# Kernel tuning notes

Hardware: AMD Instinct MI355X
Metric: run time of the kernel (lower is better)

Reference implementation:

```python
import jax, jax.numpy as jnp
import numpy as np
from jax import lax

V, E, H, B, T = 50000, 512, 512, 128, 256
OUT = 2

def gru(x, Wi, Wh, bi, bh):
    # x: [B,T,D]; PyTorch GRU equations, h0 = 0. Returns all hidden states [B,T,H].
    Bsz = x.shape[0]
    Hd = Wh.shape[1]
    xW = jnp.einsum('btd,gd->btg', x, Wi) + bi  # [B,T,3H], precompute input projections
    def step(h, xw):
        gh = h @ Wh.T + bh
        xr, xz, xn = jnp.split(xw, 3, axis=-1)
        hr, hz, hn = jnp.split(gh, 3, axis=-1)
        r = jax.nn.sigmoid(xr + hr)
        z = jax.nn.sigmoid(xz + hz)
        n = jnp.tanh(xn + r * hn)
        h_new = (1.0 - z) * n + z * h
        return h_new, h_new
    h0 = jnp.zeros((Bsz, Hd), x.dtype)
    _, hs = lax.scan(step, h0, jnp.swapaxes(xW, 0, 1))
    return jnp.swapaxes(hs, 0, 1)

def dual_attention(u, r, u_all_sum, Aw, bw, Ww):
    # u, r: [B,T,D] (query side / response side per timestep, vectorized over T).
    # w_t[b,t] = (u A^T + b) . r  (the original bmm of [B,1,D] x [B,D,1])
    w = jnp.einsum('btd,btd->bt', jnp.einsum('btd,ed->bte', u, Aw) + bw, r)
    # score = softmax over D of tanh(w) * Ww  (Linear(1, D, bias=False))
    sc = jax.nn.softmax(jnp.tanh(w)[..., None] * Ww[None, None, :], axis=-1)  # [B,T,D]
    # sum_s embed[b,s,:] * score[b,t,:] = score * (sum over time) ; then * r_t
    return sc * u_all_sum[:, None, :] * r  # [B,T,D]

def setup_inputs() -> dict:
    key = jax.random.key(0)
    ks = jax.random.split(key, 24)
    d = {}
    d['ask'] = jax.random.randint(ks[0], (B, T), 0, V, dtype=jnp.int32)
    d['answer'] = jax.random.randint(ks[1], (B, T), 0, V, dtype=jnp.int32)
    d['ask_keyword'] = jax.random.randint(ks[2], (B, T), 0, V, dtype=jnp.int32)
    d['answer_keyword'] = jax.random.randint(ks[3], (B, T), 0, V, dtype=jnp.int32)
    d['embed'] = jax.random.normal(ks[4], (V, E), jnp.float32) * 0.02
    # GRU 1: input E -> hidden H
    d['Wi1'] = jax.random.normal(ks[5], (3 * H, E), jnp.float32) * 0.05
    d['Wh1'] = jax.random.normal(ks[6], (3 * H, H), jnp.float32) * 0.05
    d['bi1'] = jnp.zeros((3 * H,), jnp.float32)
    d['bh1'] = jnp.zeros((3 * H,), jnp.float32)
    # word attention: Linear(E,E) + Linear(1,E,bias=False)
    d['Aw'] = jax.random.normal(ks[7], (E, E), jnp.float32) * 0.05
    d['bw'] = jnp.zeros((E,), jnp.float32)
    d['Ww'] = jax.random.normal(ks[8], (E,), jnp.float32) * 0.05
    # seq attention: Linear(H,H) + Linear(1,H,bias=False)
    d['As'] = jax.random.normal(ks[9], (H, H), jnp.float32) * 0.05
    d['bs'] = jnp.zeros((H,), jnp.float32)
    d['Ws'] = jax.random.normal(ks[10], (H,), jnp.float32) * 0.05
    # GRU 2: input E+H -> hidden H
    d['Wi2'] = jax.random.normal(ks[11], (3 * H, E + H), jnp.float32) * 0.05
    d['Wh2'] = jax.random.normal(ks[12], (3 * H, H), jnp.float32) * 0.05
    d['bi2'] = jnp.zeros((3 * H,), jnp.float32)
    d['bh2'] = jnp.zeros((3 * H,), jnp.float32)
    # final classifier
    d['Wf'] = jax.random.normal(ks[13], (OUT, H), jnp.float32) * 0.05
    d['bf'] = jnp.zeros((OUT,), jnp.float32)
    return d

def reference(ask, answer, ask_keyword, answer_keyword, embed, Wi1, Wh1, bi1, bh1,
              Aw, bw, Ww, As, bs, Ws, Wi2, Wh2, bi2, bh2, Wf, bf):
    ask_e = embed[ask]            # [B,T,E]
    ans_e = embed[answer]
    ask_kw = embed[ask_keyword]
    ans_kw = embed[answer_keyword]
    h_ask = gru(ask_e, Wi1, Wh1, bi1, bh1)  # [B,T,H]
    h_ans = gru(ans_e, Wi1, Wh1, bi1, bh1)
    # dual attention, vectorized over the original Python loop over t
    ctx_word = dual_attention(ask_kw, ans_kw, ask_kw.sum(axis=1), Aw, bw, Ww)   # [B,T,E]
    ctx_seq = dual_attention(h_ask, h_ans, h_ask.sum(axis=1), As, bs, Ws)       # [B,T,H]
    v = jnp.concatenate([ctx_word, ctx_seq], axis=-1)  # [B,T,E+H]
    h2 = gru(v, Wi2, Wh2, bi2, bh2)[:, -1, :]  # final hidden state [B,H]
    # dropout is identity in eval mode
    return jax.nn.softmax(h2 @ Wf.T + bf, axis=1)
```

## Files before the change

kernel.cpp:

```cpp
#include <hip/hip_runtime.h>
#include <cstdio>

typedef __bf16 bf16x8 __attribute__((ext_vector_type(8)));
typedef float f32x4 __attribute__((ext_vector_type(4)));

#define DEV __device__ __forceinline__

DEV short f2bf(float f) {
    unsigned u = __builtin_bit_cast(unsigned, f);
    u += 0x7fffu + ((u >> 16) & 1u);
    return (short)(u >> 16);
}
DEV float bf2f(short s) {
    unsigned u = ((unsigned)(unsigned short)s) << 16;
    return __builtin_bit_cast(float, u);
}
DEV float sigmoidf_(float x) { return 1.0f / (1.0f + __expf(-x)); }
DEV float tanhf_(float x) { float e = __expf(2.0f * x); return 1.0f - 2.0f / (e + 1.0f); }

DEV void gload_lds16(const void* g, void* l) {
    __builtin_amdgcn_global_load_lds(
        (__attribute__((address_space(1))) void*)(g),
        (__attribute__((address_space(3))) void*)(l), 16, 0, 0);
}

DEV f32x4 mfma16(bf16x8 a, bf16x8 b, f32x4 c) {
    return __builtin_amdgcn_mfma_f32_16x16x32_bf16(a, b, c, 0, 0, 0);
}

__global__ void f2bf_vec(const float* __restrict__ in, short* __restrict__ out, int n4) {
    int i = blockIdx.x * 256 + threadIdx.x;
    if (i >= n4) return;
    float4 v = reinterpret_cast<const float4*>(in)[i];
    short4 o;
    o.x = f2bf(v.x); o.y = f2bf(v.y); o.z = f2bf(v.z); o.w = f2bf(v.w);
    reinterpret_cast<short4*>(out)[i] = o;
}

__global__ void pack_wh(const float* __restrict__ Wh, short* __restrict__ Wp) {
    int tile = blockIdx.x, kk = blockIdx.y, l = threadIdx.x;
    int n = tile * 16 + (l & 15);
    int k0 = kk * 32 + (l >> 4) * 8;
    const float* src = Wh + (size_t)n * 512 + k0;
    short o[8];
#pragma unroll
    for (int e = 0; e < 8; e++) o[e] = f2bf(src[e]);
    *(int4*)(Wp + ((size_t)(tile * 16 + kk) * 64 + l) * 8) = *(int4*)o;
}

enum { M_XW1 = 0, M_UAW = 1, M_UAS = 2, M_XW2 = 3 };

template<int MODE>
__global__ __launch_bounds__(256) void gemm_bt(
    const short* __restrict__ Abase, const short* __restrict__ A2,
    const int* __restrict__ tok0, const int* __restrict__ tok1,
    const short* __restrict__ W, const float* __restrict__ bias,
    short* __restrict__ C, int M, int N, int K)
{
    __shared__ short Als[128 * 64];
    __shared__ short Bls[128 * 64];
    int tid = threadIdx.x;
    int m0 = blockIdx.y * 128, n0 = blockIdx.x * 128;
    int kc = (tid & 7) * 8;

    const short* arow[4];
#pragma unroll
    for (int i = 0; i < 4; i++) {
        int gm = m0 + i * 32 + (tid >> 3);
        if (MODE == M_XW1) {
            int t = gm >> 8, s = gm & 255;
            int tok = (s < 128) ? tok0[s * 256 + t] : tok1[(s - 128) * 256 + t];
            arow[i] = Abase + (size_t)tok * 512;
        } else if (MODE == M_UAW) {
            int t = gm >> 7, b = gm & 127;
            arow[i] = Abase + (size_t)tok0[b * 256 + t] * 512;
        } else if (MODE == M_UAS) {
            int t = gm >> 7, b = gm & 127;
            arow[i] = Abase + ((size_t)t * 256 + b) * 512;
        } else {
            arow[i] = Abase + (size_t)gm * 512;
        }
    }

    f32x4 acc[4][4] = {};
    int l = tid & 63, w = tid >> 6;
    int wm = (w >> 1) * 64, wn = (w & 1) * 64;

    for (int kt = 0; kt < K; kt += 64) {
#pragma unroll
        for (int i = 0; i < 4; i++) {
            const short* asrc;
            if (MODE == M_XW2) {
                int gm = m0 + i * 32 + (tid >> 3);
                const short* base = (kt < 512) ? Abase : A2;
                asrc = base + (size_t)gm * 512 + (kt & 511) + kc;
            } else {
                asrc = arow[i] + kt + kc;
            }
            gload_lds16(asrc, &Als[i * 2048 + tid * 8]);
        }
#pragma unroll
        for (int i = 0; i < 4; i++) {
            const short* bsrc = W + (size_t)(n0 + i * 32 + (tid >> 3)) * K + kt + kc;
            gload_lds16(bsrc, &Bls[i * 2048 + tid * 8]);
        }
        __syncthreads();
#pragma unroll
        for (int kk = 0; kk < 2; kk++) {
            int ko = kk * 32 + (l >> 4) * 8;
            bf16x8 af[4], bfr[4];
#pragma unroll
            for (int mi = 0; mi < 4; mi++)
                af[mi] = *(const bf16x8*)&Als[(wm + mi * 16 + (l & 15)) * 64 + ko];
#pragma unroll
            for (int ni = 0; ni < 4; ni++)
                bfr[ni] = *(const bf16x8*)&Bls[(wn + ni * 16 + (l & 15)) * 64 + ko];
#pragma unroll
            for (int mi = 0; mi < 4; mi++)
#pragma unroll
                for (int ni = 0; ni < 4; ni++)
                    acc[mi][ni] = mfma16(af[mi], bfr[ni], acc[mi][ni]);
        }
        __syncthreads();
    }
#pragma unroll
    for (int ni = 0; ni < 4; ni++) {
        int col = n0 + wn + ni * 16 + (l & 15);
        float bv = bias[col];
#pragma unroll
        for (int mi = 0; mi < 4; mi++) {
            int row0 = m0 + wm + mi * 16 + (l >> 4) * 4;
#pragma unroll
            for (int j = 0; j < 4; j++)
                C[(size_t)(row0 + j) * N + col] = f2bf(acc[mi][ni][j] + bv);
        }
    }
}

template<int WRITE_ALL>
__global__ __launch_bounds__(256, 1) void gru_scan10(
    const short* __restrict__ xW,
    const short* __restrict__ Wp,
    const float* __restrict__ bh,
    short* __restrict__ hb0, short* __restrict__ hb1,
    short* __restrict__ h_all,
    float* __restrict__ h_final,
    unsigned* __restrict__ done,
    int S, int T)
{
    __shared__ char wl[96 * 1024];
    __shared__ char sl[32 * 1024];
    __shared__ char ho[2048];

    int cb = blockIdx.x;
    int rg = blockIdx.y;
    int r0 = rg * 32;
    int tid = threadIdx.x;
    int w = tid >> 6, l = tid & 63;
    int rt = w >> 1, ct = w & 1;
    int lrow = l & 15, lq = l >> 4;
    int colg = cb * 32 + ct * 16 + lrow;
    unsigned* mydone = done + rg * 32;

    for (int rr = 0; rr < 24; rr++) {
        int flat = rr * 256 + tid;
        int lane = flat & 63, kk = (flat >> 6) & 15, lg = flat >> 10;
        int g = lg >> 1, c2 = lg & 1;
        gload_lds16(Wp + (((size_t)(g * 32 + cb * 2 + c2) * 16 + kk) * 64 + lane) * 8,
                    wl + flat * 16);
    }
    float bhv[3];
#pragma unroll
    for (int g = 0; g < 3; g++) bhv[g] = bh[g * 512 + colg];
    __syncthreads();

    float hp[4] = {};

    for (int t = 0; t < T; t++) {
        short xrv[4], xzv[4], xnv[4];
        const short* xbase = xW + ((size_t)t * S + r0) * 1536 + colg;
#pragma unroll
        for (int j = 0; j < 4; j++) {
            const short* xp = xbase + (size_t)(rt * 16 + lq * 4 + j) * 1536;
            xrv[j] = xp[0]; xzv[j] = xp[512]; xnv[j] = xp[1024];
        }

        f32x4 acc[3] = {};
        if (t > 0) {
            const short* hprev = ((t & 1) ? hb0 : hb1) + (size_t)r0 * 512;
            if (tid < 16) {
                while (__hip_atomic_load(&mydone[tid], __ATOMIC_RELAXED,
                                         __HIP_MEMORY_SCOPE_AGENT) < (unsigned)t)
                    __builtin_amdgcn_s_sleep(1);
            }
            __syncthreads();
            unsigned long long v[16];
            const unsigned long long* sp = (const unsigned long long*)hprev;
#pragma unroll
            for (int k = 0; k < 16; k++)
                v[k] = __hip_atomic_load(sp + k * 256 + tid,
                                         __ATOMIC_RELAXED, __HIP_MEMORY_SCOPE_AGENT);
#pragma unroll
            for (int k = 0; k < 16; k++) {
                int off = (k * 256 + tid) * 8;
                int row = off >> 10, colb = off & 1023;
                *(unsigned long long*)(sl + row * 1024 + (colb ^ ((row & 7) << 4))) = v[k];
            }
            __syncthreads();
            bf16x8 afr[16];
            int ar = rt * 16 + lrow;
#pragma unroll
            for (int kk = 0; kk < 16; kk++) {
                int colb = kk * 64 + lq * 16;
                afr[kk] = *(const bf16x8*)(sl + ar * 1024 + (colb ^ ((ar & 7) << 4)));
            }
#pragma unroll
            for (int g = 0; g < 3; g++) {
                const char* bbase = wl + (size_t)((g * 2 + ct) * 16) * 1024 + l * 16;
#pragma unroll
                for (int kk = 0; kk < 16; kk++) {
                    bf16x8 bfr = *(const bf16x8*)(bbase + kk * 1024);
                    acc[g] = mfma16(afr[kk], bfr, acc[g]);
                }
            }
        }

        float hv[4];
#pragma unroll
        for (int j = 0; j < 4; j++) {
            float r = sigmoidf_(bf2f(xrv[j]) + bhv[0] + acc[0][j]);
            float z = sigmoidf_(bf2f(xzv[j]) + bhv[1] + acc[1][j]);
            float n = tanhf_(bf2f(xnv[j]) + r * (acc[2][j] + bhv[2]));
            hv[j] = (1.f - z) * n + z * hp[j];
            hp[j] = hv[j];
            *(short*)(ho + (rt * 16 + lq * 4 + j) * 64 + (ct * 16 + lrow) * 2) = f2bf(hv[j]);
        }
        __syncthreads();
        {
            int row = tid >> 3, ch = tid & 7;
            unsigned long long val = *(const unsigned long long*)(ho + row * 64 + ch * 8);
            short* hnew = (t & 1) ? hb1 : hb0;
            __hip_atomic_store(
                (unsigned long long*)(hnew + (size_t)(r0 + row) * 512 + cb * 32 + ch * 4),
                val, __ATOMIC_RELAXED, __HIP_MEMORY_SCOPE_AGENT);
            if (WRITE_ALL)
                *(unsigned long long*)(h_all + ((size_t)t * S + r0 + row) * 512 + cb * 32 + ch * 4) = val;
        }
        if (!WRITE_ALL && t == T - 1) {
#pragma unroll
            for (int j = 0; j < 4; j++)
                h_final[(size_t)(r0 + rt * 16 + lq * 4 + j) * 512 + colg] = hv[j];
        }
        __syncthreads();
        if (tid == 0)
            __hip_atomic_store(&mydone[cb], (unsigned)(t + 1),
                               __ATOMIC_RELAXED, __HIP_MEMORY_SCOPE_AGENT);
    }
}

__global__ void embed_sum_k(const short* __restrict__ ebf, const int* __restrict__ tok,
                            float* __restrict__ out) {
    int b = blockIdx.x, d = threadIdx.x;
    float a0 = 0.f, a1 = 0.f;
    for (int t = 0; t < 256; t++) {
        const short* row = ebf + (size_t)tok[b * 256 + t] * 512;
        a0 += bf2f(row[d]); a1 += bf2f(row[d + 256]);
    }
    out[b * 512 + d] = a0; out[b * 512 + d + 256] = a1;
}
__global__ void hall_sum_k(const short* __restrict__ h_all, float* __restrict__ out) {
    int b = blockIdx.x, d = threadIdx.x;
    float a0 = 0.f, a1 = 0.f;
    for (int t = 0; t < 256; t++) {
        const short* row = h_all + ((size_t)t * 256 + b) * 512;
        a0 += bf2f(row[d]); a1 += bf2f(row[d + 256]);
    }
    out[b * 512 + d] = a0; out[b * 512 + d + 256] = a1;
}

template<int WORD>
__global__ __launch_bounds__(256) void attn_combine(
    const short* __restrict__ uA, const short* __restrict__ rsrc,
    const int* __restrict__ rtok, const float* __restrict__ usum,
    const float* __restrict__ Wv, short* __restrict__ ctx)
{
    int l = threadIdx.x & 63, w = threadIdx.x >> 6;
    int m = blockIdx.x * 4 + w;
    int t = m >> 7, b = m & 127;
    const short* rrow;
    if (WORD) rrow = rsrc + (size_t)rtok[b * 256 + t] * 512;
    else      rrow = rsrc + ((size_t)t * 256 + 128 + b) * 512;
    const short* urow = uA + (size_t)m * 512;
    int d0 = l * 8;
    short ru[8], uu[8];
    *(int4*)ru = *(const int4*)(rrow + d0);
    *(int4*)uu = *(const int4*)(urow + d0);
    float rv[8], dot = 0.f;
#pragma unroll
    for (int i = 0; i < 8; i++) { rv[i] = bf2f(ru[i]); dot += rv[i] * bf2f(uu[i]); }
#pragma unroll
    for (int off = 32; off >= 1; off >>= 1) dot += __shfl_xor(dot, off);
    float tw = tanhf_(dot);
    float e[8], se = 0.f;
#pragma unroll
    for (int i = 0; i < 8; i++) { e[i] = __expf(tw * Wv[d0 + i]); se += e[i]; }
#pragma unroll
    for (int off = 32; off >= 1; off >>= 1) se += __shfl_xor(se, off);
    float inv = 1.f / se;
    short ov[8];
#pragma unroll
    for (int i = 0; i < 8; i++) ov[i] = f2bf(e[i] * inv * usum[b * 512 + d0 + i] * rv[i]);
    *(int4*)(ctx + (size_t)m * 512 + d0) = *(int4*)ov;
}

__global__ void final_head_k(const float* __restrict__ h2, const float* __restrict__ Wf,
                             const float* __restrict__ bfv, float* __restrict__ out) {
    int b = blockIdx.x, l = threadIdx.x;
    float d0 = 0.f, d1 = 0.f;
    for (int k = l; k < 512; k += 64) {
        float h = h2[b * 512 + k];
        d0 += h * Wf[k];
        d1 += h * Wf[512 + k];
    }
#pragma unroll
    for (int off = 32; off >= 1; off >>= 1) { d0 += __shfl_xor(d0, off); d1 += __shfl_xor(d1, off); }
    if (l == 0) {
        float l0 = d0 + bfv[0], l1 = d1 + bfv[1];
        float mx = fmaxf(l0, l1);
        float e0 = __expf(l0 - mx), e1 = __expf(l1 - mx);
        float s = e0 + e1;
        out[b * 2] = e0 / s; out[b * 2 + 1] = e1 / s;
    }
}

extern "C" void kernel_launch(void* const* d_in, const int* in_sizes, int n_in,
                              void* d_out, int out_size, void* d_ws, size_t ws_size,
                              hipStream_t stream)
{
    const int* ask    = (const int*)d_in[0];
    const int* answer = (const int*)d_in[1];
    const int* askkw  = (const int*)d_in[2];
    const int* anskw  = (const int*)d_in[3];
    const float* embed = (const float*)d_in[4];
    const float* Wi1 = (const float*)d_in[5];
    const float* Wh1 = (const float*)d_in[6];
    const float* bi1 = (const float*)d_in[7];
    const float* bh1 = (const float*)d_in[8];
    const float* Aw  = (const float*)d_in[9];
    const float* bw  = (const float*)d_in[10];
    const float* Ww  = (const float*)d_in[11];
    const float* As  = (const float*)d_in[12];
    const float* bs  = (const float*)d_in[13];
    const float* Ws  = (const float*)d_in[14];
    const float* Wi2 = (const float*)d_in[15];
    const float* Wh2 = (const float*)d_in[16];
    const float* bi2 = (const float*)d_in[17];
    const float* bh2 = (const float*)d_in[18];
    const float* Wf  = (const float*)d_in[19];
    const float* bfv = (const float*)d_in[20];

    char* ws = (char*)d_ws;
    size_t off = 0;
    auto alloc = [&](size_t bytes) -> void* {
        void* p = (void*)(ws + off);
        off += (bytes + 255) & ~(size_t)255;
        return p;
    };
    short* embed_bf = (short*)alloc(50000ULL * 512 * 2);
    short* Wi1b = (short*)alloc(1536 * 512 * 2);
    short* Wp1  = (short*)alloc(1536 * 512 * 2);
    short* Awb  = (short*)alloc(512 * 512 * 2);
    short* Asb  = (short*)alloc(512 * 512 * 2);
    short* Wi2b = (short*)alloc(1536 * 1024 * 2);
    short* Wp2  = (short*)alloc(1536 * 512 * 2);
    char* X = (char*)alloc(201326592ULL);
    short* xW1  = (short*)X;
    short* uA   = (short*)X;
    short* ctxW = (short*)(X + 33554432);
    short* ctxS = (short*)(X + 67108864);
    short* xW2  = (short*)(X + 100663296);
    short* h_all = (short*)alloc(256ULL * 256 * 512 * 2);
    short* hb0 = (short*)alloc(256 * 512 * 2);
    short* hb1 = (short*)alloc(256 * 512 * 2);
    float* usumW = (float*)alloc(128 * 512 * 4);
    float* usumS = (float*)alloc(128 * 512 * 4);
    float* h2f   = (float*)alloc(128 * 512 * 4);
    unsigned* done1 = (unsigned*)alloc(8 * 32 * 4);
    unsigned* done2 = (unsigned*)alloc(4 * 32 * 4);

    if (off > ws_size) {
        fprintf(stderr, "kernel_launch: workspace too small: need %zu have %zu\n", off, ws_size);
        return;
    }

    hipMemsetAsync(done1, 0, 8 * 32 * 4, stream);
    hipMemsetAsync(done2, 0, 4 * 32 * 4, stream);

    auto cv = [&](const float* src, short* dst, int n) {
        int n4 = n / 4;
        f2bf_vec<<<(n4 + 255) / 256, 256, 0, stream>>>(src, dst, n4);
    };
    cv(embed, embed_bf, 50000 * 512);
    cv(Wi1, Wi1b, 1536 * 512);
    cv(Aw, Awb, 512 * 512);
    cv(As, Asb, 512 * 512);
    cv(Wi2, Wi2b, 1536 * 1024);
    pack_wh<<<dim3(96, 16), 64, 0, stream>>>(Wh1, Wp1);
    pack_wh<<<dim3(96, 16), 64, 0, stream>>>(Wh2, Wp2);

    gemm_bt<M_XW1><<<dim3(12, 512), 256, 0, stream>>>(
        embed_bf, nullptr, ask, answer, Wi1b, bi1, xW1, 65536, 1536, 512);

    {
        const short* xWa = xW1; const short* Wpa = Wp1; const float* bha = bh1;
        short* a0 = hb0; short* a1 = hb1; short* ha = h_all; float* hf = h2f;
        unsigned* dp = done1; int S = 256, T = 256;
        void* args[] = { (void*)&xWa, (void*)&Wpa, (void*)&bha, (void*)&a0, (void*)&a1,
                         (void*)&ha, (void*)&hf, (void*)&dp, (void*)&S, (void*)&T };
        hipError_t e = hipLaunchCooperativeKernel(
            reinterpret_cast<void*>(&gru_scan10<1>), dim3(16, 8), dim3(256), args, 0, stream);
        if (e != hipSuccess)
            gru_scan10<1><<<dim3(16, 8), 256, 0, stream>>>(xWa, Wpa, bha, a0, a1, ha, hf, dp, S, T);
    }

    embed_sum_k<<<128, 256, 0, stream>>>(embed_bf, askkw, usumW);
    gemm_bt<M_UAW><<<dim3(4, 256), 256, 0, stream>>>(
        embed_bf, nullptr, askkw, nullptr, Awb, bw, uA, 32768, 512, 512);
    attn_combine<1><<<8192, 256, 0, stream>>>(uA, embed_bf, anskw, usumW, Ww, ctxW);

    hall_sum_k<<<128, 256, 0, stream>>>(h_all, usumS);
    gemm_bt<M_UAS><<<dim3(4, 256), 256, 0, stream>>>(
        h_all, nullptr, nullptr, nullptr, Asb, bs, uA, 32768, 512, 512);
    attn_combine<0><<<8192, 256, 0, stream>>>(uA, h_all, nullptr, usumS, Ws, ctxS);

    gemm_bt<M_XW2><<<dim3(12, 256), 256, 0, stream>>>(
        ctxW, ctxS, nullptr, nullptr, Wi2b, bi2, xW2, 32768, 1536, 1024);

    {
        const short* xWa = xW2; const short* Wpa = Wp2; const float* bha = bh2;
        short* a0 = hb0; short* a1 = hb1; short* ha = nullptr; float* hf = h2f;
        unsigned* dp = done2; int S = 128, T = 256;
        void* args[] = { (void*)&xWa, (void*)&Wpa, (void*)&bha, (void*)&a0, (void*)&a1,
                         (void*)&ha, (void*)&hf, (void*)&dp, (void*)&S, (void*)&T };
        hipError_t e = hipLaunchCooperativeKernel(
            reinterpret_cast<void*>(&gru_scan10<0>), dim3(16, 4), dim3(256), args, 0, stream);
        if (e != hipSuccess)
            gru_scan10<0><<<dim3(16, 4), 256, 0, stream>>>(xWa, Wpa, bha, a0, a1, ha, hf, dp, S, T);
    }

    final_head_k<<<128, 64, 0, stream>>>(h2f, Wf, bfv, (float*)d_out);
}
```

Baseline: 2.227 ms.

## Fuse input-projection GEMMs and attention into persistent GRU scan kernels

Result: faster. 1.930 ms, median of 2 (-13.3%).

```diff
diff --git a/kernel.cpp b/kernel.cpp
--- a/kernel.cpp
+++ b/kernel.cpp
@@ -23,9 +23,23 @@
         (__attribute__((address_space(1))) void*)(g),
         (__attribute__((address_space(3))) void*)(l), 16, 0, 0);
 }
-
 DEV f32x4 mfma16(bf16x8 a, bf16x8 b, f32x4 c) {
     return __builtin_amdgcn_mfma_f32_16x16x32_bf16(a, b, c, 0, 0, 0);
+}
+DEV unsigned ald(const unsigned* p) {
+    return __hip_atomic_load(p, __ATOMIC_RELAXED, __HIP_MEMORY_SCOPE_AGENT);
+}
+DEV unsigned long long ald64(const void* p) {
+    return __hip_atomic_load((const unsigned long long*)p, __ATOMIC_RELAXED, __HIP_MEMORY_SCOPE_AGENT);
+}
+DEV void ast64(void* p, unsigned long long v) {
+    __hip_atomic_store((unsigned long long*)p, v, __ATOMIC_RELAXED, __HIP_MEMORY_SCOPE_AGENT);
+}
+DEV void ast32(void* p, unsigned v) {
+    __hip_atomic_store((unsigned*)p, v, __ATOMIC_RELAXED, __HIP_MEMORY_SCOPE_AGENT);
+}
+DEV void aadd(unsigned* p, unsigned v) {
+    __hip_atomic_fetch_add(p, v, __ATOMIC_RELAXED, __HIP_MEMORY_SCOPE_AGENT);
 }
 
 __global__ void f2bf_vec(const float* __restrict__ in, short* __restrict__ out, int n4) {
@@ -48,33 +62,31 @@
     *(int4*)(Wp + ((size_t)(tile * 16 + kk) * 64 + l) * 8) = *(int4*)o;
 }
 
-enum { M_XW1 = 0, M_UAW = 1, M_UAS = 2, M_XW2 = 3 };
+enum { A_XW1 = 0, A_UAW = 1, A_UAS = 2, A_XW2 = 3 };
 
 template<int MODE>
-__global__ __launch_bounds__(256) void gemm_bt(
-    const short* __restrict__ Abase, const short* __restrict__ A2,
-    const int* __restrict__ tok0, const int* __restrict__ tok1,
-    const short* __restrict__ W, const float* __restrict__ bias,
-    short* __restrict__ C, int M, int N, int K)
+DEV void gemm_tile(short* Als, short* Bls, short* Ct, int m0, int n0,
+                   const short* Abase, const short* A2,
+                   const int* tok0, const int* tok1,
+                   const short* W, const float* bias, short* C, int N, int K)
 {
-    __shared__ short Als[128 * 64];
-    __shared__ short Bls[128 * 64];
     int tid = threadIdx.x;
-    int m0 = blockIdx.y * 128, n0 = blockIdx.x * 128;
+    int l = tid & 63, w = tid >> 6;
+    int wm = (w >> 1) * 64, wn = (w & 1) * 64;
     int kc = (tid & 7) * 8;
 
     const short* arow[4];
 #pragma unroll
     for (int i = 0; i < 4; i++) {
         int gm = m0 + i * 32 + (tid >> 3);
-        if (MODE == M_XW1) {
+        if (MODE == A_XW1) {
             int t = gm >> 8, s = gm & 255;
             int tok = (s < 128) ? tok0[s * 256 + t] : tok1[(s - 128) * 256 + t];
             arow[i] = Abase + (size_t)tok * 512;
-        } else if (MODE == M_UAW) {
+        } else if (MODE == A_UAW) {
             int t = gm >> 7, b = gm & 127;
             arow[i] = Abase + (size_t)tok0[b * 256 + t] * 512;
-        } else if (MODE == M_UAS) {
+        } else if (MODE == A_UAS) {
             int t = gm >> 7, b = gm & 127;
             arow[i] = Abase + ((size_t)t * 256 + b) * 512;
         } else {
@@ -83,27 +95,23 @@
     }
 
     f32x4 acc[4][4] = {};
-    int l = tid & 63, w = tid >> 6;
-    int wm = (w >> 1) * 64, wn = (w & 1) * 64;
-
     for (int kt = 0; kt < K; kt += 64) {
 #pragma unroll
         for (int i = 0; i < 4; i++) {
             const short* asrc;
-            if (MODE == M_XW2) {
+            if (MODE == A_XW2) {
                 int gm = m0 + i * 32 + (tid >> 3);
                 const short* base = (kt < 512) ? Abase : A2;
                 asrc = base + (size_t)gm * 512 + (kt & 511) + kc;
             } else {
                 asrc = arow[i] + kt + kc;
             }
-            gload_lds16(asrc, &Als[i * 2048 + tid * 8]);
-        }
-#pragma unroll
-        for (int i = 0; i < 4; i++) {
-            const short* bsrc = W + (size_t)(n0 + i * 32 + (tid >> 3)) * K + kt + kc;
-            gload_lds16(bsrc, &Bls[i * 2048 + tid * 8]);
-        }
+            gload_lds16(asrc, Als + i * 2048 + tid * 8);
+        }
+#pragma unroll
+        for (int i = 0; i < 4; i++)
+            gload_lds16(W + (size_t)(n0 + i * 32 + (tid >> 3)) * K + kt + kc,
+                        Bls + i * 2048 + tid * 8);
         __syncthreads();
 #pragma unroll
         for (int kk = 0; kk < 2; kk++) {
@@ -125,37 +133,101 @@
     }
 #pragma unroll
     for (int ni = 0; ni < 4; ni++) {
-        int col = n0 + wn + ni * 16 + (l & 15);
-        float bv = bias[col];
-#pragma unroll
-        for (int mi = 0; mi < 4; mi++) {
-            int row0 = m0 + wm + mi * 16 + (l >> 4) * 4;
-#pragma unroll
-            for (int j = 0; j < 4; j++)
-                C[(size_t)(row0 + j) * N + col] = f2bf(acc[mi][ni][j] + bv);
-        }
+        float bv = bias[n0 + wn + ni * 16 + (l & 15)];
+#pragma unroll
+        for (int mi = 0; mi < 4; mi++)
+#pragma unroll
+            for (int jj = 0; jj < 4; jj++)
+                Ct[(wm + mi * 16 + (l >> 4) * 4 + jj) * 132 + wn + ni * 16 + (l & 15)] =
+                    f2bf(acc[mi][ni][jj] + bv);
+    }
+    __syncthreads();
+    for (int r = 0; r < 16; r++) {
+        int idx = r * 256 + tid;
+        int row = idx >> 5, cc = idx & 31;
+        unsigned long long val = *(const unsigned long long*)(Ct + row * 132 + cc * 4);
+        ast64(C + (size_t)(m0 + row) * N + n0 + cc * 4, val);
+    }
+    __syncthreads();
+}
+
+DEV void embed_sum_dev(const short* ebf, const int* tok, float* out, int b) {
+    int d = threadIdx.x;
+    float a0 = 0.f, a1 = 0.f;
+    for (int t = 0; t < 256; t++) {
+        const short* row = ebf + (size_t)tok[b * 256 + t] * 512;
+        a0 += bf2f(row[d]); a1 += bf2f(row[d + 256]);
+    }
+    ast32(&out[b * 512 + d], __builtin_bit_cast(unsigned, a0));
+    ast32(&out[b * 512 + d + 256], __builtin_bit_cast(unsigned, a1));
+}
+DEV void hall_sum_dev(const short* h_all, float* out, int b) {
+    int d = threadIdx.x;
+    float a0 = 0.f, a1 = 0.f;
+    for (int t = 0; t < 256; t++) {
+        const short* row = h_all + ((size_t)t * 256 + b) * 512;
+        a0 += bf2f(row[d]); a1 += bf2f(row[d + 256]);
+    }
+    ast32(&out[b * 512 + d], __builtin_bit_cast(unsigned, a0));
+    ast32(&out[b * 512 + d + 256], __builtin_bit_cast(unsigned, a1));
+}
+
+template<int WORD, int COHOUT>
+DEV void combine4(int bb, const short* uA, const short* rsrc, const int* rtok,
+                  const float* usum, const float* Wv, short* ctx)
+{
+    int l = threadIdx.x & 63, w = threadIdx.x >> 6;
+    int m = bb * 4 + w;
+    int t = m >> 7, b = m & 127;
+    const short* rrow;
+    if (WORD) rrow = rsrc + (size_t)rtok[b * 256 + t] * 512;
+    else      rrow = rsrc + ((size_t)t * 256 + 128 + b) * 512;
+    int d0 = l * 8;
+    short ru[8], uu[8];
+    *(int4*)ru = *(const int4*)(rrow + d0);
+    *(unsigned long long*)uu       = ald64(uA + (size_t)m * 512 + d0);
+    *((unsigned long long*)uu + 1) = ald64(uA + (size_t)m * 512 + d0 + 4);
+    float rv[8], dot = 0.f;
+#pragma unroll
+    for (int i = 0; i < 8; i++) { rv[i] = bf2f(ru[i]); dot += rv[i] * bf2f(uu[i]); }
+#pragma unroll
+    for (int off = 32; off >= 1; off >>= 1) dot += __shfl_xor(dot, off);
+    float tw = tanhf_(dot);
+    float us[8];
+#pragma unroll
+    for (int i = 0; i < 4; i++) {
+        unsigned long long uv = ald64(usum + b * 512 + d0 + i * 2);
+        us[i * 2]     = __builtin_bit_cast(float, (unsigned)(uv & 0xffffffffu));
+        us[i * 2 + 1] = __builtin_bit_cast(float, (unsigned)(uv >> 32));
+    }
+    float e[8], se = 0.f;
+#pragma unroll
+    for (int i = 0; i < 8; i++) { e[i] = __expf(tw * Wv[d0 + i]); se += e[i]; }
+#pragma unroll
+    for (int off = 32; off >= 1; off >>= 1) se += __shfl_xor(se, off);
+    float inv = 1.f / se;
+    short ov[8];
+#pragma unroll
+    for (int i = 0; i < 8; i++) ov[i] = f2bf(e[i] * inv * us[i] * rv[i]);
+    if (COHOUT) {
+        ast64(ctx + (size_t)m * 512 + d0,     *(unsigned long long*)ov);
+        ast64(ctx + (size_t)m * 512 + d0 + 4, *((unsigned long long*)ov + 1));
+    } else {
+        *(int4*)(ctx + (size_t)m * 512 + d0) = *(int4*)ov;
     }
 }
 
 template<int WRITE_ALL>
-__global__ __launch_bounds__(256, 1) void gru_scan10(
-    const short* __restrict__ xW,
-    const short* __restrict__ Wp,
-    const float* __restrict__ bh,
-    short* __restrict__ hb0, short* __restrict__ hb1,
-    short* __restrict__ h_all,
-    float* __restrict__ h_final,
-    unsigned* __restrict__ done,
-    int S, int T)
+DEV void scan_role(char* smem, int cb, int rg,
+                   const short* xW, const short* Wp, const float* bh,
+                   short* hb0, short* hb1, short* h_all, float* h_final,
+                   unsigned* done, unsigned* slice_cnt, int tps, int S, int T)
 {
-    __shared__ char wl[96 * 1024];
-    __shared__ char sl[32 * 1024];
-    __shared__ char ho[2048];
-
-    int cb = blockIdx.x;
-    int rg = blockIdx.y;
+    char* wl = smem;
+    char* sl = smem + 98304;
+    char* ho = smem + 131072;
+    int tid = threadIdx.x;
     int r0 = rg * 32;
-    int tid = threadIdx.x;
     int w = tid >> 6, l = tid & 63;
     int rt = w >> 1, ct = w & 1;
     int lrow = l & 15, lq = l >> 4;
@@ -177,6 +249,14 @@
     float hp[4] = {};
 
     for (int t = 0; t < T; t++) {
+        if (tid < 16) {
+            if (t > 0)
+                while (ald(&mydone[tid]) < (unsigned)t) __builtin_amdgcn_s_sleep(1);
+        } else if (tid == 16) {
+            while (ald(&slice_cnt[t]) < (unsigned)tps) __builtin_amdgcn_s_sleep(1);
+        }
+        __syncthreads();
+
         short xrv[4], xzv[4], xnv[4];
         const short* xbase = xW + ((size_t)t * S + r0) * 1536 + colg;
 #pragma unroll
@@ -188,18 +268,11 @@
         f32x4 acc[3] = {};
         if (t > 0) {
             const short* hprev = ((t & 1) ? hb0 : hb1) + (size_t)r0 * 512;
-            if (tid < 16) {
-                while (__hip_atomic_load(&mydone[tid], __ATOMIC_RELAXED,
-                                         __HIP_MEMORY_SCOPE_AGENT) < (unsigned)t)
-                    __builtin_amdgcn_s_sleep(1);
-            }
-            __syncthreads();
             unsigned long long v[16];
             const unsigned long long* sp = (const unsigned long long*)hprev;
 #pragma unroll
             for (int k = 0; k < 16; k++)
-                v[k] = __hip_atomic_load(sp + k * 256 + tid,
-                                         __ATOMIC_RELAXED, __HIP_MEMORY_SCOPE_AGENT);
+                v[k] = ald64(sp + k * 256 + tid);
 #pragma unroll
             for (int k = 0; k < 16; k++) {
                 int off = (k * 256 + tid) * 8;
@@ -233,16 +306,14 @@
             float n = tanhf_(bf2f(xnv[j]) + r * (acc[2][j] + bhv[2]));
             hv[j] = (1.f - z) * n + z * hp[j];
             hp[j] = hv[j];
-            *(short*)(ho + (rt * 16 + lq * 4 + j) * 64 + (ct * 16 + lrow) * 2) = f2bf(hv[j]);
+            *(short*)(ho + (rt * 16 + lq * 4 + j) * 72 + (ct * 16 + lrow) * 2) = f2bf(hv[j]);
         }
         __syncthreads();
         {
             int row = tid >> 3, ch = tid & 7;
-            unsigned long long val = *(const unsigned long long*)(ho + row * 64 + ch * 8);
+            unsigned long long val = *(const unsigned long long*)(ho + row * 72 + ch * 8);
             short* hnew = (t & 1) ? hb1 : hb0;
-            __hip_atomic_store(
-                (unsigned long long*)(hnew + (size_t)(r0 + row) * 512 + cb * 32 + ch * 4),
-                val, __ATOMIC_RELAXED, __HIP_MEMORY_SCOPE_AGENT);
+            ast64(hnew + (size_t)(r0 + row) * 512 + cb * 32 + ch * 4, val);
             if (WRITE_ALL)
                 *(unsigned long long*)(h_all + ((size_t)t * S + r0 + row) * 512 + cb * 32 + ch * 4) = val;
         }
@@ -253,64 +324,102 @@
         }
         __syncthreads();
         if (tid == 0)
-            __hip_atomic_store(&mydone[cb], (unsigned)(t + 1),
-                               __ATOMIC_RELAXED, __HIP_MEMORY_SCOPE_AGENT);
-    }
-}
-
-__global__ void embed_sum_k(const short* __restrict__ ebf, const int* __restrict__ tok,
-                            float* __restrict__ out) {
-    int b = blockIdx.x, d = threadIdx.x;
-    float a0 = 0.f, a1 = 0.f;
-    for (int t = 0; t < 256; t++) {
-        const short* row = ebf + (size_t)tok[b * 256 + t] * 512;
-        a0 += bf2f(row[d]); a1 += bf2f(row[d + 256]);
-    }
-    out[b * 512 + d] = a0; out[b * 512 + d + 256] = a1;
-}
-__global__ void hall_sum_k(const short* __restrict__ h_all, float* __restrict__ out) {
-    int b = blockIdx.x, d = threadIdx.x;
-    float a0 = 0.f, a1 = 0.f;
-    for (int t = 0; t < 256; t++) {
-        const short* row = h_all + ((size_t)t * 256 + b) * 512;
-        a0 += bf2f(row[d]); a1 += bf2f(row[d + 256]);
-    }
-    out[b * 512 + d] = a0; out[b * 512 + d + 256] = a1;
-}
-
-template<int WORD>
-__global__ __launch_bounds__(256) void attn_combine(
-    const short* __restrict__ uA, const short* __restrict__ rsrc,
-    const int* __restrict__ rtok, const float* __restrict__ usum,
-    const float* __restrict__ Wv, short* __restrict__ ctx)
+            ast32(&mydone[cb], (unsigned)(t + 1));
+    }
+}
+
+__global__ __launch_bounds__(256, 1) void gru_fused1(
+    short* xW1, const short* __restrict__ Wp, const float* __restrict__ bh,
+    short* __restrict__ hb0, short* __restrict__ hb1, short* __restrict__ h_all,
+    unsigned* done, unsigned* slc,
+    const short* __restrict__ embed_bf, const int* __restrict__ ask,
+    const int* __restrict__ answer, const short* __restrict__ Wi1b,
+    const float* __restrict__ bi1,
+    const int* __restrict__ askkw, const int* __restrict__ anskw,
+    const short* __restrict__ Awb, const float* __restrict__ bw,
+    float* usumW, short* uAb, const float* __restrict__ Ww, short* ctxW,
+    unsigned* wcnt)
 {
-    int l = threadIdx.x & 63, w = threadIdx.x >> 6;
-    int m = blockIdx.x * 4 + w;
-    int t = m >> 7, b = m & 127;
-    const short* rrow;
-    if (WORD) rrow = rsrc + (size_t)rtok[b * 256 + t] * 512;
-    else      rrow = rsrc + ((size_t)t * 256 + 128 + b) * 512;
-    const short* urow = uA + (size_t)m * 512;
-    int d0 = l * 8;
-    short ru[8], uu[8];
-    *(int4*)ru = *(const int4*)(rrow + d0);
-    *(int4*)uu = *(const int4*)(urow + d0);
-    float rv[8], dot = 0.f;
-#pragma unroll
-    for (int i = 0; i < 8; i++) { rv[i] = bf2f(ru[i]); dot += rv[i] * bf2f(uu[i]); }
-#pragma unroll
-    for (int off = 32; off >= 1; off >>= 1) dot += __shfl_xor(dot, off);
-    float tw = tanhf_(dot);
-    float e[8], se = 0.f;
-#pragma unroll
-    for (int i = 0; i < 8; i++) { e[i] = __expf(tw * Wv[d0 + i]); se += e[i]; }
-#pragma unroll
-    for (int off = 32; off >= 1; off >>= 1) se += __shfl_xor(se, off);
-    float inv = 1.f / se;
-    short ov[8];
-#pragma unroll
-    for (int i = 0; i < 8; i++) ov[i] = f2bf(e[i] * inv * usum[b * 512 + d0 + i] * rv[i]);
-    *(int4*)(ctx + (size_t)m * 512 + d0) = *(int4*)ov;
+    __shared__ char smem[133376];
+    int bid = blockIdx.x, tid = threadIdx.x;
+
+    if (bid >= 128) {
+        int pid = bid - 128;
+        short* Als = (short*)smem;
+        short* Bls = (short*)(smem + 16384);
+        short* Ct  = (short*)(smem + 32768);
+        for (int q = pid; q < 256 * 24; q += 128) {
+            int slice = q / 24, j = q % 24;
+            int m0 = (slice * 2 + (j >= 12 ? 1 : 0)) * 128, n0 = (j % 12) * 128;
+            gemm_tile<A_XW1>(Als, Bls, Ct, m0, n0, embed_bf, nullptr, ask, answer,
+                             Wi1b, bi1, xW1, 1536, 512);
+            if (tid == 0) aadd(&slc[slice], 1u);
+        }
+        embed_sum_dev(embed_bf, askkw, usumW, pid);
+        for (int k = 0; k < 8; k++) {
+            int q = pid + k * 128;
+            gemm_tile<A_UAW>(Als, Bls, Ct, (q >> 2) * 128, (q & 3) * 128,
+                             embed_bf, nullptr, askkw, nullptr, Awb, bw, uAb, 512, 512);
+        }
+        if (tid == 0) {
+            aadd(wcnt, 1u);
+            while (ald(wcnt) < 128u) __builtin_amdgcn_s_sleep(1);
+        }
+        __syncthreads();
+        for (int bb = pid * 64; bb < pid * 64 + 64; bb++)
+            combine4<1, 0>(bb, uAb, embed_bf, anskw, usumW, Ww, ctxW);
+        return;
+    }
+    scan_role<1>(smem, bid & 15, bid >> 4, xW1, Wp, bh, hb0, hb1, h_all, nullptr,
+                 done, slc, 24, 256, 256);
+}
+
+__global__ __launch_bounds__(256, 1) void gru_fused2(
+    short* xW2, const short* __restrict__ Wp, const float* __restrict__ bh,
+    short* __restrict__ hb0, short* __restrict__ hb1, float* __restrict__ h_final,
+    unsigned* done, unsigned* slc,
+    const short* __restrict__ h_all, float* usumS, short* uAb,
+    const short* __restrict__ Asb, const float* __restrict__ bs,
+    const float* __restrict__ Ws, short* ctxS, const short* __restrict__ ctxW,
+    const short* __restrict__ Wi2b, const float* __restrict__ bi2,
+    unsigned* acnt, unsigned* ccnt)
+{
+    __shared__ char smem[133376];
+    int bid = blockIdx.x, tid = threadIdx.x;
+    short* Als = (short*)smem;
+    short* Bls = (short*)(smem + 16384);
+    short* Ct  = (short*)(smem + 32768);
+
+    if (bid < 128) hall_sum_dev(h_all, usumS, bid);
+    for (int k = 0; k < 4; k++) {
+        int q = bid + k * 256;
+        gemm_tile<A_UAS>(Als, Bls, Ct, (q >> 2) * 128, (q & 3) * 128,
+                         h_all, nullptr, nullptr, nullptr, Asb, bs, uAb, 512, 512);
+    }
+    if (tid == 0) {
+        aadd(acnt, 1u);
+        while (ald(acnt) < 256u) __builtin_amdgcn_s_sleep(1);
+    }
+    __syncthreads();
+    for (int bb = bid * 32; bb < bid * 32 + 32; bb++)
+        combine4<0, 1>(bb, uAb, h_all, nullptr, usumS, Ws, ctxS);
+    __syncthreads();
+    if (tid == 0) aadd(ccnt, 1u);
+
+    if (bid >= 64) {
+        int pid = bid - 64;
+        if (tid == 0) { while (ald(ccnt) < 256u) __builtin_amdgcn_s_sleep(1); }
+        __syncthreads();
+        for (int q = pid; q < 256 * 12; q += 192) {
+            int slice = q / 12, j = q % 12;
+            gemm_tile<A_XW2>(Als, Bls, Ct, slice * 128, j * 128,
+                             ctxW, ctxS, nullptr, nullptr, Wi2b, bi2, xW2, 1536, 1024);
+            if (tid == 0) aadd(&slc[slice], 1u);
+        }
+        return;
+    }
+    scan_role<0>(smem, bid & 15, bid >> 4, xW2, Wp, bh, hb0, hb1, nullptr, h_final,
+                 done, slc, 12, 128, 256);
 }
 
 __global__ void final_head_k(const float* __restrict__ h2, const float* __restrict__ Wf,
@@ -375,26 +484,31 @@
     short* Wp2  = (short*)alloc(1536 * 512 * 2);
     char* X = (char*)alloc(201326592ULL);
     short* xW1  = (short*)X;
-    short* uA   = (short*)X;
-    short* ctxW = (short*)(X + 33554432);
-    short* ctxS = (short*)(X + 67108864);
-    short* xW2  = (short*)(X + 100663296);
+    short* xW2  = (short*)X;
+    short* ctxS = (short*)(X + 100663296);
+    short* uAb  = (short*)alloc(32768ULL * 512 * 2);
+    short* ctxW = (short*)alloc(32768ULL * 512 * 2);
     short* h_all = (short*)alloc(256ULL * 256 * 512 * 2);
     short* hb0 = (short*)alloc(256 * 512 * 2);
     short* hb1 = (short*)alloc(256 * 512 * 2);
     float* usumW = (float*)alloc(128 * 512 * 4);
     float* usumS = (float*)alloc(128 * 512 * 4);
     float* h2f   = (float*)alloc(128 * 512 * 4);
-    unsigned* done1 = (unsigned*)alloc(8 * 32 * 4);
-    unsigned* done2 = (unsigned*)alloc(4 * 32 * 4);
+    unsigned* syncb = (unsigned*)alloc((8 * 32 + 4 * 32 + 256 + 256 + 96) * 4);
+    unsigned* done1 = syncb;
+    unsigned* done2 = syncb + 8 * 32;
+    unsigned* slc1  = syncb + 12 * 32;
+    unsigned* slc2  = slc1 + 256;
+    unsigned* wcnt1 = slc2 + 256;
+    unsigned* acnt2 = wcnt1 + 32;
+    unsigned* ccnt2 = wcnt1 + 64;
 
     if (off > ws_size) {
         fprintf(stderr, "kernel_launch: workspace too small: need %zu have %zu\n", off, ws_size);
         return;
     }
 
-    hipMemsetAsync(done1, 0, 8 * 32 * 4, stream);
-    hipMemsetAsync(done2, 0, 4 * 32 * 4, stream);
+    hipMemsetAsync(syncb, 0, (8 * 32 + 4 * 32 + 256 + 256 + 96) * 4, stream);
 
     auto cv = [&](const float* src, short* dst, int n) {
         int n4 = n / 4;
@@ -408,44 +522,33 @@
     pack_wh<<<dim3(96, 16), 64, 0, stream>>>(Wh1, Wp1);
     pack_wh<<<dim3(96, 16), 64, 0, stream>>>(Wh2, Wp2);
 
-    gemm_bt<M_XW1><<<dim3(12, 512), 256, 0, stream>>>(
-        embed_bf, nullptr, ask, answer, Wi1b, bi1, xW1, 65536, 1536, 512);
-
     {
-        const short* xWa = xW1; const short* Wpa = Wp1; const float* bha = bh1;
-        short* a0 = hb0; short* a1 = hb1; short* ha = h_all; float* hf = h2f;
-        unsigned* dp = done1; int S = 256, T = 256;
-        void* args[] = { (void*)&xWa, (void*)&Wpa, (void*)&bha, (void*)&a0, (void*)&a1,
-                         (void*)&ha, (void*)&hf, (void*)&dp, (void*)&S, (void*)&T };
+        void* args[] = { (void*)&xW1, (void*)&Wp1, (void*)&bh1, (void*)&hb0, (void*)&hb1,
+                         (void*)&h_all, (void*)&done1, (void*)&slc1,
+                         (void*)&embed_bf, (void*)&ask, (void*)&answer, (void*)&Wi1b, (void*)&bi1,
+                         (void*)&askkw, (void*)&anskw, (void*)&Awb, (void*)&bw,
+                         (void*)&usumW, (void*)&uAb, (void*)&Ww, (void*)&ctxW, (void*)&wcnt1 };
         hipError_t e = hipLaunchCooperativeKernel(
-            reinterpret_cast<void*>(&gru_scan10<1>), dim3(16, 8), dim3(256), args, 0, stream);
+            reinterpret_cast<void*>(&gru_fused1), dim3(256), dim3(256), args, 0, stream);
         if (e != hipSuccess)
-            gru_scan10<1><<<dim3(16, 8), 256, 0, stream>>>(xWa, Wpa, bha, a0, a1, ha, hf, dp, S, T);
-    }
-
-    embed_sum_k<<<128, 256, 0, stream>>>(embed_bf, askkw, usumW);
-    gemm_bt<M_UAW><<<dim3(4, 256), 256, 0, stream>>>(
-        embed_bf, nullptr, askkw, nullptr, Awb, bw, uA, 32768, 512, 512);
-    attn_combine<1><<<8192, 256, 0, stream>>>(uA, embed_bf, anskw, usumW, Ww, ctxW);
-
-    hall_sum_k<<<128, 256, 0, stream>>>(h_all, usumS);
-    gemm_bt<M_UAS><<<dim3(4, 256), 256, 0, stream>>>(
-        h_all, nullptr, nullptr, nullptr, Asb, bs, uA, 32768, 512, 512);
-    attn_combine<0><<<8192, 256, 0, stream>>>(uA, h_all, nullptr, usumS, Ws, ctxS);
-
-    gemm_bt<M_XW2><<<dim3(12, 256), 256, 0, stream>>>(
-        ctxW, ctxS, nullptr, nullptr, Wi2b, bi2, xW2, 32768, 1536, 1024);
+            gru_fused1<<<256, 256, 0, stream>>>(
+                xW1, Wp1, bh1, hb0, hb1, h_all, done1, slc1,
+                embed_bf, ask, answer, Wi1b, bi1,
+                askkw, anskw, Awb, bw, usumW, uAb, Ww, ctxW, wcnt1);
+    }
 
     {
-        const short* xWa = xW2; const short* Wpa = Wp2; const float* bha = bh2;
-        short* a0 = hb0; short* a1 = hb1; short* ha = nullptr; float* hf = h2f;
-        unsigned* dp = done2; int S = 128, T = 256;
-        void* args[] = { (void*)&xWa, (void*)&Wpa, (void*)&bha, (void*)&a0, (void*)&a1,
-                         (void*)&ha, (void*)&hf, (void*)&dp, (void*)&S, (void*)&T };
+        void* args[] = { (void*)&xW2, (void*)&Wp2, (void*)&bh2, (void*)&hb0, (void*)&hb1,
+                         (void*)&h2f, (void*)&done2, (void*)&slc2,
+                         (void*)&h_all, (void*)&usumS, (void*)&uAb,
+                         (void*)&Asb, (void*)&bs, (void*)&Ws, (void*)&ctxS, (void*)&ctxW,
+                         (void*)&Wi2b, (void*)&bi2, (void*)&acnt2, (void*)&ccnt2 };
         hipError_t e = hipLaunchCooperativeKernel(
-            reinterpret_cast<void*>(&gru_scan10<0>), dim3(16, 4), dim3(256), args, 0, stream);
+            reinterpret_cast<void*>(&gru_fused2), dim3(256), dim3(256), args, 0, stream);
         if (e != hipSuccess)
-            gru_scan10<0><<<dim3(16, 4), 256, 0, stream>>>(xWa, Wpa, bha, a0, a1, ha, hf, dp, S, T);
+            gru_fused2<<<256, 256, 0, stream>>>(
+                xW2, Wp2, bh2, hb0, hb1, h2f, done2, slc2,
+                h_all, usumS, uAb, Asb, bs, Ws, ctxS, ctxW, Wi2b, bi2, acnt2, ccnt2);
     }
 
     final_head_k<<<128, 64, 0, stream>>>(h2f, Wf, bfv, (float*)d_out);
```
